# Performance work log

Hardware: AMD Instinct MI355X
Metric: run time of the kernel (lower is better)

The kernel has to match this reference:

```python
import jax, jax.numpy as jnp
import numpy as np

DEPTH, HEADS, DIM_HEAD = 6, 8, 32
D_MODEL, D_FF = 256, 1024
B, N, D_IN, N_CLS = 4, 4096, 128, 10
NB_FEAT = int(DIM_HEAD * np.log(DIM_HEAD))  # 110 random features (performer_pytorch default)


def _ortho_gaussian(m, d, rng):
    # gaussian orthogonal random projection (FAVOR+), rows rescaled by chi-distributed norms
    blocks = []
    for _ in range(int(np.ceil(m / d))):
        q, _ = np.linalg.qr(rng.standard_normal((d, d)))
        blocks.append(q.T)
    mat = np.concatenate(blocks, 0)[:m]
    mult = np.linalg.norm(rng.standard_normal((m, d)), axis=1)
    return (mult[:, None] * mat).astype(np.float32)


def setup_inputs() -> dict:
    rng = np.random.default_rng(0)
    w = lambda *s: jnp.asarray((rng.standard_normal(s) * 0.02).astype(np.float32))
    z = lambda *s: jnp.zeros(s, jnp.float32)
    o = lambda *s: jnp.ones(s, jnp.float32)
    proj = jnp.asarray(np.stack([_ortho_gaussian(NB_FEAT, DIM_HEAD, rng) for _ in range(DEPTH)]))
    return dict(
        x=jnp.asarray(rng.standard_normal((B, N, D_IN)).astype(np.float32)),
        mask=jnp.ones((B, N), bool),
        w_in=w(D_IN, D_MODEL), b_in=z(D_MODEL),
        ln1_g=o(DEPTH, D_MODEL), ln1_b=z(DEPTH, D_MODEL),
        wq=w(DEPTH, D_MODEL, D_MODEL), wk=w(DEPTH, D_MODEL, D_MODEL),
        wv=w(DEPTH, D_MODEL, D_MODEL), wo=w(DEPTH, D_MODEL, D_MODEL), bo=z(DEPTH, D_MODEL),
        proj=proj,
        ln2_g=o(DEPTH, D_MODEL), ln2_b=z(DEPTH, D_MODEL),
        w1=w(DEPTH, D_MODEL, D_FF), b1=z(DEPTH, D_FF),
        w2=w(DEPTH, D_FF, D_MODEL), b2=z(DEPTH, D_MODEL),
        cls_g=o(D_MODEL), cls_b=z(D_MODEL),
        wc1=w(D_MODEL, D_MODEL), bc1=z(D_MODEL),
        wc2=w(D_MODEL, N_CLS), bc2=z(N_CLS),
    )


def _ln(x, g, b, eps=1e-5):
    mu = x.mean(-1, keepdims=True)
    var = ((x - mu) ** 2).mean(-1, keepdims=True)
    return (x - mu) * jax.lax.rsqrt(var + eps) * g + b


def _softmax_kernel(data, proj, is_query, eps=1e-4):
    # FAVOR+ positive softmax features (performer_pytorch softmax_kernel)
    dn = data.shape[-1] ** -0.25
    ratio = proj.shape[0] ** -0.5
    dd = jnp.einsum('bhnd,md->bhnm', data * dn, proj)
    diag = 0.5 * (dn ** 2) * jnp.sum(data ** 2, axis=-1, keepdims=True)  # [B,H,N,1]
    if is_query:
        m = jnp.max(dd, axis=-1, keepdims=True)
    else:
        m = jnp.max(dd, axis=(-2, -1), keepdims=True)
    m = jax.lax.stop_gradient(m)
    return ratio * (jnp.exp(dd - diag - m) + eps)


def _linear_attn(q, k, v):
    # non-causal O(n) attention: q,k [B,H,N,M], v [B,H,N,dh]
    k_sum = k.sum(-2)                                            # [B,H,M]
    d_inv = 1.0 / jnp.einsum('bhnm,bhm->bhn', q, k_sum)          # [B,H,N]
    ctx = jnp.einsum('bhnm,bhnd->bhmd', k, v)                    # [B,H,M,dh]
    return jnp.einsum('bhnm,bhmd,bhn->bhnd', q, ctx, d_inv)


def _forward(x, mask, w_in, b_in, ln1_g, ln1_b, wq, wk, wv, wo, bo, proj,
             ln2_g, ln2_b, w1, b1, w2, b2, cls_g, cls_b, wc1, bc1, wc2, bc2):
    b_, n_ = x.shape[:2]
    h = x @ w_in + b_in
    mb = mask[:, None, :, None]
    split = lambda t: t.reshape(b_, n_, HEADS, DIM_HEAD).transpose(0, 2, 1, 3)
    for i in range(DEPTH):
        y = _ln(h, ln1_g[i], ln1_b[i])
        q, k, v = split(y @ wq[i]), split(y @ wk[i]), split(y @ wv[i])
        v = jnp.where(mb, v, 0.0)
        qp = _softmax_kernel(q, proj[i], True)
        kp = _softmax_kernel(k, proj[i], False)
        a = _linear_attn(qp, kp, v).transpose(0, 2, 1, 3).reshape(b_, n_, D_MODEL)
        h = h + a @ wo[i] + bo[i]
        y2 = _ln(h, ln2_g[i], ln2_b[i])
        h = h + jax.nn.gelu(y2 @ w1[i] + b1[i], approximate=False) @ w2[i] + b2[i]
    p = h.mean(1)
    z = jax.nn.relu(_ln(p, cls_g, cls_b))
    z = jax.nn.relu(z @ wc1 + bc1)
    return z @ wc2 + bc2


def reference(x, mask, w_in, b_in, ln1_g, ln1_b, wq, wk, wv, wo, bo, proj,
              ln2_g, ln2_b, w1, b1, w2, b2, cls_g, cls_b, wc1, bc1, wc2, bc2):
    return _forward(x, mask, w_in, b_in, ln1_g, ln1_b, wq, wk, wv, wo, bo, proj,
                    ln2_g, ln2_b, w1, b1, w2, b2, cls_g, cls_b, wc1, bc1, wc2, bc2)
```

## Files before the change

### kernel.cpp

```cpp
#include <hip/hip_runtime.h>
#include <cstdint>
#include <cstddef>

typedef __attribute__((ext_vector_type(8))) short bf16x8;
typedef __attribute__((ext_vector_type(4))) float f32x4;
typedef unsigned short u16;
typedef unsigned int u32;

static constexpr float DN    = 0.42044820762685725f;
static constexpr float DN2   = 0.17677669529663687f;
static constexpr float RATIO = 0.09534625892455924f;
static constexpr float KEPS  = 1e-4f;

__device__ __forceinline__ float b2f(u16 u) {
    union { float f; u32 i; } x; x.i = ((u32)u) << 16; return x.f;
}
__device__ __forceinline__ u16 f2b(float f) {
    union { float f; u32 i; } x; x.f = f;
    u32 r = (x.i + 0x7FFFu + ((x.i >> 16) & 1u)) >> 16;
    return (u16)r;
}
__device__ __forceinline__ float wred_sum(float v) {
#pragma unroll
    for (int o = 32; o > 0; o >>= 1) v += __shfl_xor(v, o, 64);
    return v;
}
__device__ __forceinline__ float gelu_f(float v) {
    return 0.5f * v * (1.f + erff(v * 0.7071067811865475f));
}
__device__ __forceinline__ void gload16(const u16* g, u16* l) {
    __builtin_amdgcn_global_load_lds(
        (const __attribute__((address_space(1))) u32*)(const u32*)g,
        (__attribute__((address_space(3))) u32*)(u32*)l, 16, 0, 0);
}

__global__ __launch_bounds__(256) void trk(const float* __restrict__ src, u16* __restrict__ dst,
                                           int K, int N)
{
    const size_t bo = (size_t)blockIdx.z * K * N;
    src += bo; dst += bo;
    __shared__ float tl[32][33];
    const int t = threadIdx.x, tx = t & 31, ty = t >> 5;
    const int k0 = blockIdx.y * 32, n0 = blockIdx.x * 32;
#pragma unroll
    for (int p = 0; p < 4; ++p)
        tl[ty + p * 8][tx] = src[(size_t)(k0 + ty + p * 8) * N + n0 + tx];
    __syncthreads();
#pragma unroll
    for (int p = 0; p < 4; ++p)
        dst[(size_t)(n0 + ty + p * 8) * K + k0 + tx] = f2b(tl[tx][ty + p * 8]);
}

__global__ __launch_bounds__(256) void xcast(const float* __restrict__ x, u16* __restrict__ xb)
{
    const int i = blockIdx.x * 256 + threadIdx.x;
    const float4 v = ((const float4*)x)[i];
    uint2 r;
    r.x = (u32)f2b(v.x) | ((u32)f2b(v.y) << 16);
    r.y = (u32)f2b(v.z) | ((u32)f2b(v.w) << 16);
    ((uint2*)xb)[i] = r;
}

template<int CMODE, int NP, bool QKV, bool AHEAD, bool CHEAD>
__global__ __launch_bounds__(512) void gemm3(
    const u16* __restrict__ A, const u16* __restrict__ Bt,
    const float* __restrict__ bias, u16* __restrict__ Cb, int ldc,
    u16* __restrict__ hres, const float* __restrict__ lng, const float* __restrict__ lnb,
    u16* __restrict__ yout, int K, int lda, int nrt)
{
    constexpr int KC    = (NP == 128) ? 256 : 128;
    constexpr int SLOTS = KC / 8;
    constexpr int SSH   = (SLOTS == 32) ? 5 : 4;
    constexpr int BB    = NP * KC * 2;
    constexpr int ABYT  = 64 * KC * 2;
    constexpr int NCB   = NP / 128;
    constexpr int EPI   = (CMODE <= 1) ? (64 * 136 * 2) : (64 * 264 * 2 + 4608);
    __shared__ __align__(16) char smem[BB + 2 * ABYT + EPI];
    u16*  Bs   = (u16*)smem;
    u16*  Asm  = (u16*)(smem + BB);
    char* epi  = smem + BB + 2 * ABYT;

    const u16* Btl = Bt;
    u16* Cbl = Cb;
    if (QKV) { Btl += (size_t)blockIdx.z * 393216; Cbl += (size_t)blockIdx.z * 4194304; }
    const int t = threadIdx.x, w = t >> 6, lr = (t & 63) & 15, lg = (t & 63) >> 4;
    const int p = blockIdx.x;
    const int NC = K / KC;

    auto STAGE_B = [&](int c) {
#pragma unroll
        for (int i = 0; i < BB / 16 / 512; ++i) {
            const int u = i * 512 + t;
            const int col = u >> SSH, slot = u & (SLOTS - 1);
            const int gs = slot ^ (col & 7);
            gload16(Btl + (size_t)(p * NP + col) * K + c * KC + gs * 8, Bs + u * 8);
        }
    };
    auto STAGE_A = [&](int c, int row0, int buf) {
        u16* dst = Asm + buf * (ABYT / 2);
#pragma unroll
        for (int i = 0; i < ABYT / 16 / 512; ++i) {
            const int u = i * 512 + t;
            const int row = u >> SSH, slot = u & (SLOTS - 1);
            const int gs = slot ^ (row & 7);
            const u16* src;
            if (AHEAD) {
                const int kg = c * KC + gs * 8;
                src = A + ((size_t)((row0 >> 12) * 8 + (kg >> 5)) * 4096 + (row0 & 4095) + row) * 32 + (kg & 31);
            } else {
                src = A + (size_t)(row0 + row) * lda + c * KC + gs * 8;
            }
            gload16(src, dst + u * 8);
        }
    };

    f32x4 acc[4][NCB];
    auto ZERO = [&]() {
#pragma unroll
        for (int i = 0; i < 4; ++i)
#pragma unroll
            for (int j = 0; j < NCB; ++j) acc[i][j] = f32x4{0.f, 0.f, 0.f, 0.f};
    };
    auto KLOOP = [&](int buf) {
        const u16* Ac = Asm + buf * (ABYT / 2);
#pragma unroll
        for (int ks = 0; ks < KC / 32; ++ks) {
            bf16x8 af[4], bfv[NCB];
#pragma unroll
            for (int rbk = 0; rbk < 4; ++rbk) {
                const int row = rbk * 16 + lr;
                af[rbk] = *(const bf16x8*)&Ac[row * KC + (((ks * 4 + lg) ^ (row & 7)) << 3)];
            }
#pragma unroll
            for (int cb = 0; cb < NCB; ++cb) {
                const int col = w * (NP / 8) + cb * 16 + lr;
                bfv[cb] = *(const bf16x8*)&Bs[col * KC + (((ks * 4 + lg) ^ (col & 7)) << 3)];
            }
#pragma unroll
            for (int rbk = 0; rbk < 4; ++rbk)
#pragma unroll
                for (int cb = 0; cb < NCB; ++cb)
                    acc[rbk][cb] = __builtin_amdgcn_mfma_f32_16x16x32_bf16(af[rbk], bfv[cb], acc[rbk][cb], 0, 0, 0);
        }
    };

    auto EPILOGUE = [&](int row0) {
        if constexpr (CMODE <= 1) {
            u16* ctile = (u16*)epi;
            float bv[NCB];
#pragma unroll
            for (int cb = 0; cb < NCB; ++cb) {
                const int col = p * NP + w * (NP / 8) + cb * 16 + lr;
                bv[cb] = bias ? bias[col] : 0.f;
            }
#pragma unroll
            for (int rbk = 0; rbk < 4; ++rbk)
#pragma unroll
                for (int cb = 0; cb < NCB; ++cb)
#pragma unroll
                    for (int rr = 0; rr < 4; ++rr) {
                        const int rl = rbk * 16 + 4 * lg + rr;
                        float v = acc[rbk][cb][rr] + bv[cb];
                        if (CMODE == 1) v = gelu_f(v);
                        ctile[rl * 136 + w * (NP / 8) + cb * 16 + lr] = f2b(v);
                    }
            __syncthreads();
            if constexpr (CHEAD) {
                const int bq = row0 >> 12, n0 = row0 & 4095;
#pragma unroll
                for (int i = 0; i < 2; ++i) {
                    const int u = i * 512 + t;
                    const int hh = u >> 8, rem = u & 255;
                    const int row = rem >> 2, dblk = rem & 3;
                    *(uint4*)(Cbl + ((size_t)(bq * 8 + p * 4 + hh) * 4096 + n0 + row) * 32 + dblk * 8)
                        = *(const uint4*)&ctile[row * 136 + hh * 32 + dblk * 8];
                }
            } else {
#pragma unroll
                for (int i = 0; i < 2; ++i) {
                    const int u = i * 512 + t;
                    const int row = u >> 4, seg = u & 15;
                    *(uint4*)(Cbl + (size_t)(row0 + row) * ldc + p * 128 + seg * 8)
                        = *(const uint4*)&ctile[row * 136 + seg * 8];
                }
            }
        } else {
            u16*   ctile = (u16*)epi;
            float* rsum  = (float*)(epi + 33792);
            float* rsum2 = rsum + 512;
            float* rmu   = rsum2 + 512;
            float* rrs   = rmu + 64;
            int cidx[NCB]; float bv[NCB];
#pragma unroll
            for (int cb = 0; cb < NCB; ++cb) {
                cidx[cb] = w * 32 + cb * 16 + lr;
                bv[cb] = bias ? bias[cidx[cb]] : 0.f;
            }
            if constexpr (CMODE == 2 || CMODE == 4) {
#pragma unroll
                for (int i = 0; i < 4; ++i) {
                    const int u = i * 512 + t;
                    const int row = u >> 5, seg = u & 31;
                    *(uint4*)&ctile[row * 264 + seg * 8]
                        = *(const uint4*)(hres + (size_t)(row0 + row) * 256 + seg * 8);
                }
                __syncthreads();
            }
#pragma unroll
            for (int rbk = 0; rbk < 4; ++rbk)
#pragma unroll
                for (int cb = 0; cb < NCB; ++cb)
#pragma unroll
                    for (int rr = 0; rr < 4; ++rr) {
                        const int rl = rbk * 16 + 4 * lg + rr;
                        float v = acc[rbk][cb][rr] + bv[cb];
                        if constexpr (CMODE == 2 || CMODE == 4)
                            v += b2f(ctile[rl * 264 + cidx[cb]]);
                        acc[rbk][cb][rr] = v;
                    }
            __syncthreads();
            if constexpr (CMODE != 4) {
#pragma unroll
                for (int rbk = 0; rbk < 4; ++rbk)
#pragma unroll
                    for (int rr = 0; rr < 4; ++rr) {
                        float s1 = acc[rbk][0][rr] + acc[rbk][NCB - 1][rr];
                        float s2 = fmaf(acc[rbk][0][rr], acc[rbk][0][rr],
                                        acc[rbk][NCB - 1][rr] * acc[rbk][NCB - 1][rr]);
#pragma unroll
                        for (int off = 1; off < 16; off <<= 1) {
                            s1 += __shfl_xor(s1, off, 64);
                            s2 += __shfl_xor(s2, off, 64);
                        }
                        if (lr == 0) {
                            const int rl = rbk * 16 + 4 * lg + rr;
                            rsum[rl * 8 + w] = s1; rsum2[rl * 8 + w] = s2;
                        }
                    }
                __syncthreads();
                if (t < 64) {
                    float s1 = 0.f, s2 = 0.f;
#pragma unroll
                    for (int j = 0; j < 8; ++j) { s1 += rsum[t * 8 + j]; s2 += rsum2[t * 8 + j]; }
                    const float mu = s1 * (1.f / 256.f);
                    const float var = s2 * (1.f / 256.f) - mu * mu;
                    rmu[t] = mu; rrs[t] = rsqrtf(var + 1e-5f);
                }
                __syncthreads();
            }
#pragma unroll
            for (int rbk = 0; rbk < 4; ++rbk)
#pragma unroll
                for (int cb = 0; cb < NCB; ++cb)
#pragma unroll
                    for (int rr = 0; rr < 4; ++rr) {
                        const int rl = rbk * 16 + 4 * lg + rr;
                        ctile[rl * 264 + cidx[cb]] = f2b(acc[rbk][cb][rr]);
                    }
            __syncthreads();
#pragma unroll
            for (int i = 0; i < 4; ++i) {
                const int u = i * 512 + t;
                const int row = u >> 5, seg = u & 31;
                *(uint4*)(hres + (size_t)(row0 + row) * 256 + seg * 8)
                    = *(const uint4*)&ctile[row * 264 + seg * 8];
            }
            if constexpr (CMODE != 4) {
                __syncthreads();
                float gv[NCB], bb2[NCB];
#pragma unroll
                for (int cb = 0; cb < NCB; ++cb) { gv[cb] = lng[cidx[cb]]; bb2[cb] = lnb[cidx[cb]]; }
#pragma unroll
                for (int rbk = 0; rbk < 4; ++rbk)
#pragma unroll
                    for (int cb = 0; cb < NCB; ++cb)
#pragma unroll
                        for (int rr = 0; rr < 4; ++rr) {
                            const int rl = rbk * 16 + 4 * lg + rr;
                            const float yv = (acc[rbk][cb][rr] - rmu[rl]) * rrs[rl] * gv[cb] + bb2[cb];
                            ctile[rl * 264 + cidx[cb]] = f2b(yv);
                        }
                __syncthreads();
#pragma unroll
                for (int i = 0; i < 4; ++i) {
                    const int u = i * 512 + t;
                    const int row = u >> 5, seg = u & 31;
                    *(uint4*)(yout + (size_t)(row0 + row) * 256 + seg * 8)
                        = *(const uint4*)&ctile[row * 264 + seg * 8];
                }
            }
        }
    };

    if (NC == 1) {
        int ab = 0;
        STAGE_B(0);
        STAGE_A(0, blockIdx.y * nrt * 64, 0);
        asm volatile("s_waitcnt vmcnt(0)" ::: "memory");
        __syncthreads();
        for (int rt = 0; rt < nrt; ++rt) {
            const int row0 = (blockIdx.y * nrt + rt) * 64;
            if (rt + 1 < nrt) STAGE_A(0, row0 + 64, ab ^ 1);
            ZERO();
            KLOOP(ab);
            EPILOGUE(row0);
            asm volatile("s_waitcnt vmcnt(0)" ::: "memory");
            __syncthreads();
            ab ^= 1;
        }
    } else {
        const int row0 = blockIdx.y * 64;
        ZERO();
        for (int c = 0; c < NC; ++c) {
            if (c) __syncthreads();
            STAGE_B(c);
            STAGE_A(c, row0, 0);
            asm volatile("s_waitcnt vmcnt(0)" ::: "memory");
            __syncthreads();
            KLOOP(0);
        }
        EPILOGUE(row0);
    }
}

__global__ __launch_bounds__(256) void kctx2(
    const u16* __restrict__ kg, const u16* __restrict__ vg,
    const float* __restrict__ proj, float* __restrict__ ctxp, float* __restrict__ Mcp,
    float* __restrict__ vsump)
{
    __shared__ __align__(16) u16 projS[112 * 32];
    __shared__ __align__(16) u16 kS[128 * 32];
    __shared__ __align__(16) u16 vTS[48 * 128];
    __shared__ __align__(16) u16 eTS[112 * 128];
    __shared__ float diagS[128];
    __shared__ float redS[4];
    const int t = threadIdx.x, w = t >> 6, lane = t & 63, lr = lane & 15, lg = lane >> 4;
    const int bh = blockIdx.x >> 3, chunk = blockIdx.x & 7;

    for (int idx = t; idx < 112 * 32; idx += 256) {
        const int m = idx >> 5, d = idx & 31;
        projS[idx] = (m < 110) ? f2b(proj[m * 32 + d] * DN) : (u16)0;
    }
    for (int idx = t; idx < 16 * 128; idx += 256) {
        const int rr = idx >> 7;
        vTS[(32 + rr) * 128 + (idx & 127)] = (rr == 0) ? f2b(1.0f) : (u16)0;
    }
    for (int idx = t; idx < 16 * 128; idx += 256)
        eTS[112 * 128 + idx] = 0;

    f32x4 E[2][3];
#pragma unroll
    for (int i = 0; i < 2; ++i)
#pragma unroll
        for (int j = 0; j < 3; ++j) E[i][j] = f32x4{0.f, 0.f, 0.f, 0.f};
    float Mrun = -INFINITY;
    float vsAcc = 0.f;

    for (int r = 0; r < 4; ++r) {
        const size_t eb = ((size_t)bh * 4096 + chunk * 512 + r * 128) * 32;
#pragma unroll
        for (int i = 0; i < 2; ++i) {
            const int u = i * 256 + t;
            ((uint4*)kS)[u] = ((const uint4*)(kg + eb))[u];
        }
#pragma unroll
        for (int i = 0; i < 2; ++i) {
            const int u = i * 256 + t;
            const int tok = u >> 2, dblk = u & 3;
            union { uint4 v; u16 s[8]; } uu;
            uu.v = ((const uint4*)(vg + eb))[u];
#pragma unroll
            for (int j = 0; j < 8; ++j) {
                const int d = dblk * 8 + j;
                vTS[d * 128 + ((((tok >> 3) ^ (d & 15))) << 3) + (tok & 7)] = uu.s[j];
            }
        }
        __syncthreads();
        {
            const int d = t >> 3, seg = t & 7;
            union { uint4 v; u16 s[8]; } ua, ub;
            ua.v = *(const uint4*)&vTS[d * 128 + seg * 16];
            ub.v = *(const uint4*)&vTS[d * 128 + seg * 16 + 8];
            float s = 0.f;
#pragma unroll
            for (int j = 0; j < 8; ++j) s += b2f(ua.s[j]) + b2f(ub.s[j]);
            vsAcc += s;
        }
        if (t < 128) {
            float s = 0.f;
#pragma unroll
            for (int dq = 0; dq < 4; ++dq) {
                union { uint4 v; u16 ss[8]; } uu;
                uu.v = ((const uint4*)kS)[t * 4 + dq];
#pragma unroll
                for (int j = 0; j < 8; ++j) { const float f = b2f(uu.ss[j]); s = fmaf(f, f, s); }
            }
            diagS[t] = 0.5f * DN2 * s;
        }
        __syncthreads();
        f32x4 dd[7][2];
#pragma unroll
        for (int mb = 0; mb < 7; ++mb)
#pragma unroll
            for (int tb = 0; tb < 2; ++tb) dd[mb][tb] = f32x4{0.f, 0.f, 0.f, 0.f};
        bf16x8 kf[2];
#pragma unroll
        for (int tb = 0; tb < 2; ++tb)
            kf[tb] = *(const bf16x8*)&kS[(w * 32 + tb * 16 + lr) * 32 + lg * 8];
#pragma unroll
        for (int mb = 0; mb < 7; ++mb) {
            const bf16x8 pf = *(const bf16x8*)&projS[(mb * 16 + lr) * 32 + lg * 8];
#pragma unroll
            for (int tb = 0; tb < 2; ++tb)
                dd[mb][tb] = __builtin_amdgcn_mfma_f32_16x16x32_bf16(pf, kf[tb], dd[mb][tb], 0, 0, 0);
        }
        float mx = -INFINITY;
#pragma unroll
        for (int mb = 0; mb < 7; ++mb)
#pragma unroll
            for (int tb = 0; tb < 2; ++tb)
#pragma unroll
                for (int rr = 0; rr < 4; ++rr) {
                    if (mb == 6 && (4 * lg + rr) >= 14) continue;
                    mx = fmaxf(mx, dd[mb][tb][rr]);
                }
#pragma unroll
        for (int off = 1; off < 64; off <<= 1) mx = fmaxf(mx, __shfl_xor(mx, off, 64));
        if (lane == 0) redS[w] = mx;
        __syncthreads();
        float Mnew = fmaxf(fmaxf(redS[0], redS[1]), fmaxf(redS[2], redS[3]));
        Mnew = fmaxf(Mrun, Mnew);
        const float scl = __expf(Mrun - Mnew);
#pragma unroll
        for (int i = 0; i < 2; ++i)
#pragma unroll
            for (int j = 0; j < 3; ++j)
#pragma unroll
                for (int rr = 0; rr < 4; ++rr) E[i][j][rr] *= scl;
        Mrun = Mnew;
        const float dg0 = diagS[w * 32 + lr], dg1 = diagS[w * 32 + 16 + lr];
#pragma unroll
        for (int mb = 0; mb < 7; ++mb)
#pragma unroll
            for (int tb = 0; tb < 2; ++tb)
#pragma unroll
                for (int rr = 0; rr < 4; ++rr) {
                    const int tok = w * 32 + tb * 16 + lr;
                    const int m = mb * 16 + 4 * lg + rr;
                    const float e = __expf(dd[mb][tb][rr] - (tb ? dg1 : dg0) - Mnew);
                    eTS[m * 128 + ((((tok >> 3) ^ (m & 15))) << 3) + (tok & 7)] = f2b(e);
                }
        __syncthreads();
#pragma unroll
        for (int ks = 0; ks < 4; ++ks) {
            bf16x8 aF[2], bF[3];
#pragma unroll
            for (int mb2 = 0; mb2 < 2; ++mb2) {
                const int m = w * 32 + mb2 * 16 + lr;
                aF[mb2] = *(const bf16x8*)&eTS[m * 128 + (((ks * 4 + lg) ^ lr) << 3)];
            }
#pragma unroll
            for (int nb = 0; nb < 3; ++nb) {
                const int d = nb * 16 + lr;
                bF[nb] = *(const bf16x8*)&vTS[d * 128 + (((ks * 4 + lg) ^ lr) << 3)];
            }
#pragma unroll
            for (int mb2 = 0; mb2 < 2; ++mb2)
#pragma unroll
                for (int nb = 0; nb < 3; ++nb)
                    E[mb2][nb] = __builtin_amdgcn_mfma_f32_16x16x32_bf16(aF[mb2], bF[nb], E[mb2][nb], 0, 0, 0);
        }
        __syncthreads();
    }
    const size_t ob = (size_t)blockIdx.x * 112 * 33;
#pragma unroll
    for (int mb2 = 0; mb2 < 2; ++mb2)
#pragma unroll
        for (int nb = 0; nb < 3; ++nb)
#pragma unroll
            for (int rr = 0; rr < 4; ++rr) {
                const int m = w * 32 + mb2 * 16 + 4 * lg + rr;
                if (m < 112) {
                    if (nb < 2) ctxp[ob + m * 33 + nb * 16 + lr] = E[mb2][nb][rr];
                    else if (lr == 0) ctxp[ob + m * 33 + 32] = E[mb2][nb][rr];
                }
            }
    if (t == 0) Mcp[blockIdx.x] = Mrun;
    float vs = vsAcc;
#pragma unroll
    for (int o = 4; o > 0; o >>= 1) vs += __shfl_xor(vs, o, 64);
    if ((t & 7) == 0) vsump[blockIdx.x * 32 + (t >> 3)] = vs;
}

__global__ __launch_bounds__(256) void kred2(
    const float* __restrict__ ctxp, const float* __restrict__ Mcp,
    const float* __restrict__ vsump,
    u16* __restrict__ ctxTg, float* __restrict__ ksumg)
{
    __shared__ float vsumS[32];
    __shared__ float wS[8];
    const int t = threadIdx.x, bh = blockIdx.x;
    float M = -INFINITY;
#pragma unroll
    for (int c = 0; c < 8; ++c) M = fmaxf(M, Mcp[bh * 8 + c]);
    if (t < 8) wS[t] = __expf(Mcp[bh * 8 + t] - M);
    if (t < 32) {
        float s = 0.f;
#pragma unroll
        for (int c = 0; c < 8; ++c) s += vsump[(bh * 8 + c) * 32 + t];
        vsumS[t] = s;
    }
    __syncthreads();
    for (int idx = t; idx < 4096; idx += 256) {
        const int d = idx >> 7, m = idx & 127;
        float val = 0.f;
        if (m < 110) {
            float s = 0.f;
#pragma unroll
            for (int c = 0; c < 8; ++c)
                s += wS[c] * ctxp[((size_t)(bh * 8 + c) * 112 + m) * 33 + d];
            val = RATIO * (s + KEPS * vsumS[d]);
        }
        ctxTg[(size_t)bh * 4096 + idx] = f2b(val);
    }
    if (t < 128) {
        float val = 0.f;
        if (t < 110) {
            float s = 0.f;
#pragma unroll
            for (int c = 0; c < 8; ++c)
                s += wS[c] * ctxp[((size_t)(bh * 8 + c) * 112 + t) * 33 + 32];
            val = RATIO * (s + KEPS * 4096.0f);
        }
        ksumg[bh * 128 + t] = val;
    }
}

__global__ __launch_bounds__(256) void qattn2(
    const u16* __restrict__ qg, const float* __restrict__ proj,
    const u16* __restrict__ ctxTg, const float* __restrict__ ksumg, u16* __restrict__ ag)
{
    __shared__ __align__(16) u16 projS[112 * 32];
    __shared__ __align__(16) u16 qS[128 * 32];
    __shared__ __align__(16) u16 ctxTS[32 * 128];
    __shared__ __align__(16) u16 pS[128 * 128];
    __shared__ float ksumS[128], diagS[128], dinvS[128];
    const int t = threadIdx.x, w = t >> 6, lr = (t & 63) & 15, lg = (t & 63) >> 4;
    const int bh = blockIdx.x >> 5, chunk = blockIdx.x & 31;

    for (int idx = t; idx < 112 * 32; idx += 256) {
        const int m = idx >> 5, d = idx & 31;
        projS[idx] = (m < 110) ? f2b(proj[m * 32 + d] * DN) : (u16)0;
    }
#pragma unroll
    for (int i = 0; i < 2; ++i) {
        const int u = i * 256 + t;
        const int d = u >> 4, s = u & 15;
        *(uint4*)&ctxTS[d * 128 + (((s ^ (d & 15))) << 3)] =
            *(const uint4*)(ctxTg + (size_t)bh * 4096 + d * 128 + s * 8);
    }
    if (t < 128) ksumS[t] = ksumg[bh * 128 + t];
    const size_t qeb = ((size_t)bh * 4096 + chunk * 128) * 32;
#pragma unroll
    for (int i = 0; i < 2; ++i) {
        const int u = i * 256 + t;
        ((uint4*)qS)[u] = ((const uint4*)(qg + qeb))[u];
    }
    {
        const int tok = t >> 1, s = 14 + (t & 1);
        *(uint4*)&pS[tok * 128 + (((s ^ (tok & 15))) << 3)] = uint4{0, 0, 0, 0};
    }
    __syncthreads();
    if (t < 128) {
        float s = 0.f;
#pragma unroll
        for (int dq = 0; dq < 4; ++dq) {
            union { uint4 v; u16 ss[8]; } uu;
            uu.v = ((const uint4*)qS)[t * 4 + dq];
#pragma unroll
            for (int j = 0; j < 8; ++j) { const float f = b2f(uu.ss[j]); s = fmaf(f, f, s); }
        }
        diagS[t] = 0.5f * DN2 * s;
    }
    __syncthreads();
    f32x4 dd[7][2];
#pragma unroll
    for (int mb = 0; mb < 7; ++mb)
#pragma unroll
        for (int tb = 0; tb < 2; ++tb) dd[mb][tb] = f32x4{0.f, 0.f, 0.f, 0.f};
    bf16x8 qf[2];
#pragma unroll
    for (int tb = 0; tb < 2; ++tb)
        qf[tb] = *(const bf16x8*)&qS[(w * 32 + tb * 16 + lr) * 32 + lg * 8];
#pragma unroll
    for (int mb = 0; mb < 7; ++mb) {
        const bf16x8 pf = *(const bf16x8*)&projS[(mb * 16 + lr) * 32 + lg * 8];
#pragma unroll
        for (int tb = 0; tb < 2; ++tb)
            dd[mb][tb] = __builtin_amdgcn_mfma_f32_16x16x32_bf16(pf, qf[tb], dd[mb][tb], 0, 0, 0);
    }
    float mx[2], den[2];
#pragma unroll
    for (int tb = 0; tb < 2; ++tb) {
        float v = -INFINITY;
#pragma unroll
        for (int mb = 0; mb < 7; ++mb)
#pragma unroll
            for (int rr = 0; rr < 4; ++rr) {
                if (mb == 6 && (4 * lg + rr) >= 14) continue;
                v = fmaxf(v, dd[mb][tb][rr]);
            }
        v = fmaxf(v, __shfl_xor(v, 16, 64));
        v = fmaxf(v, __shfl_xor(v, 32, 64));
        mx[tb] = v;
        den[tb] = 0.f;
    }
    const float dg0 = diagS[w * 32 + lr], dg1 = diagS[w * 32 + 16 + lr];
#pragma unroll
    for (int mb = 0; mb < 7; ++mb)
#pragma unroll
        for (int tb = 0; tb < 2; ++tb)
#pragma unroll
            for (int rr = 0; rr < 4; ++rr) {
                const int m = mb * 16 + 4 * lg + rr;
                const int tok = w * 32 + tb * 16 + lr;
                const float pv = RATIO * (__expf(dd[mb][tb][rr] - (tb ? dg1 : dg0) - mx[tb]) + KEPS);
                den[tb] += pv * ksumS[m];
                pS[tok * 128 + ((((m >> 3) ^ (tok & 15))) << 3) + (m & 7)] = f2b(pv);
            }
#pragma unroll
    for (int tb = 0; tb < 2; ++tb) {
        den[tb] += __shfl_xor(den[tb], 16, 64);
        den[tb] += __shfl_xor(den[tb], 32, 64);
        if (lg == 0) dinvS[w * 32 + tb * 16 + lr] = 1.f / den[tb];
    }
    __syncthreads();
    f32x4 o[2][2];
#pragma unroll
    for (int i = 0; i < 2; ++i)
#pragma unroll
        for (int j = 0; j < 2; ++j) o[i][j] = f32x4{0.f, 0.f, 0.f, 0.f};
#pragma unroll
    for (int ks = 0; ks < 4; ++ks) {
        bf16x8 aF[2], bF[2];
#pragma unroll
        for (int tb = 0; tb < 2; ++tb) {
            const int tok = w * 32 + tb * 16 + lr;
            aF[tb] = *(const bf16x8*)&pS[tok * 128 + (((ks * 4 + lg) ^ lr) << 3)];
        }
#pragma unroll
        for (int nb = 0; nb < 2; ++nb) {
            const int d = nb * 16 + lr;
            bF[nb] = *(const bf16x8*)&ctxTS[d * 128 + (((ks * 4 + lg) ^ lr) << 3)];
        }
#pragma unroll
        for (int tb = 0; tb < 2; ++tb)
#pragma unroll
            for (int nb = 0; nb < 2; ++nb)
                o[tb][nb] = __builtin_amdgcn_mfma_f32_16x16x32_bf16(aF[tb], bF[nb], o[tb][nb], 0, 0, 0);
    }
    u16* outS = qS;
#pragma unroll
    for (int tb = 0; tb < 2; ++tb)
#pragma unroll
        for (int nb = 0; nb < 2; ++nb)
#pragma unroll
            for (int rr = 0; rr < 4; ++rr) {
                const int tokl = w * 32 + tb * 16 + 4 * lg + rr;
                outS[tokl * 32 + nb * 16 + lr] = f2b(o[tb][nb][rr] * dinvS[tokl]);
            }
    __syncthreads();
#pragma unroll
    for (int i = 0; i < 2; ++i) {
        const int u = i * 256 + t;
        ((uint4*)(ag + qeb))[u] = ((const uint4*)outS)[u];
    }
}

__global__ __launch_bounds__(256) void pool_k(const u16* __restrict__ h,
                                              float* __restrict__ pp)
{
    const int b = blockIdx.x, ch = blockIdx.y, d = threadIdx.x;
    const u16* p = h + ((size_t)b * 4096 + ch * 256) * 256 + d;
    float s = 0.f;
    for (int n = 0; n < 256; ++n) s += b2f(p[(size_t)n * 256]);
    pp[(b * 16 + ch) * 256 + d] = s;
}

__global__ __launch_bounds__(256) void cls_k(const float* __restrict__ pp,
                                             const float* __restrict__ g,
                                             const float* __restrict__ bb,
                                             const float* __restrict__ wc1,
                                             const float* __restrict__ bc1,
                                             const float* __restrict__ wc2,
                                             const float* __restrict__ bc2,
                                             float* __restrict__ out)
{
    __shared__ float pS[4][256];
    __shared__ float zS[4][256];
    __shared__ float z2S[4][256];
    const int t = threadIdx.x;
#pragma unroll
    for (int b = 0; b < 4; ++b) {
        float s = 0.f;
        for (int c = 0; c < 16; ++c) s += pp[(b * 16 + c) * 256 + t];
        pS[b][t] = s * (1.f / 4096.f);
    }
    __syncthreads();
    {
        const int w = t >> 6, lane = t & 63;
        const float4 v = *reinterpret_cast<const float4*>(&pS[w][lane * 4]);
        float s = v.x + v.y + v.z + v.w;
        float ss = fmaf(v.x, v.x, fmaf(v.y, v.y, fmaf(v.z, v.z, v.w * v.w)));
        s = wred_sum(s); ss = wred_sum(ss);
        const float mu = s * (1.f / 256.f);
        const float var = ss * (1.f / 256.f) - mu * mu;
        const float rr = rsqrtf(var + 1e-5f);
        const float4 gv = *reinterpret_cast<const float4*>(g + lane * 4);
        const float4 bv = *reinterpret_cast<const float4*>(bb + lane * 4);
        zS[w][lane * 4 + 0] = fmaxf((v.x - mu) * rr * gv.x + bv.x, 0.f);
        zS[w][lane * 4 + 1] = fmaxf((v.y - mu) * rr * gv.y + bv.y, 0.f);
        zS[w][lane * 4 + 2] = fmaxf((v.z - mu) * rr * gv.z + bv.z, 0.f);
        zS[w][lane * 4 + 3] = fmaxf((v.w - mu) * rr * gv.w + bv.w, 0.f);
    }
    __syncthreads();
#pragma unroll
    for (int b = 0; b < 4; ++b) {
        float s = bc1[t];
        for (int j = 0; j < 256; ++j) s = fmaf(zS[b][j], wc1[j * 256 + t], s);
        z2S[b][t] = fmaxf(s, 0.f);
    }
    __syncthreads();
    if (t < 40) {
        const int b = t / 10, c = t % 10;
        float s = bc2[c];
        for (int j = 0; j < 256; ++j) s = fmaf(z2S[b][j], wc2[j * 10 + c], s);
        out[t] = s;
    }
}

extern "C" void kernel_launch(void* const* d_in, const int* in_sizes, int n_in,
                              void* d_out, int out_size, void* d_ws, size_t ws_size,
                              hipStream_t stream)
{
    const float* x    = (const float*)d_in[0];
    const float* w_in = (const float*)d_in[2];
    const float* b_in = (const float*)d_in[3];
    const float* ln1g = (const float*)d_in[4];
    const float* ln1b = (const float*)d_in[5];
    const float* wq   = (const float*)d_in[6];
    const float* wk   = (const float*)d_in[7];
    const float* wv   = (const float*)d_in[8];
    const float* wo   = (const float*)d_in[9];
    const float* bo   = (const float*)d_in[10];
    const float* proj = (const float*)d_in[11];
    const float* ln2g = (const float*)d_in[12];
    const float* ln2b = (const float*)d_in[13];
    const float* w1   = (const float*)d_in[14];
    const float* b1   = (const float*)d_in[15];
    const float* w2   = (const float*)d_in[16];
    const float* b2   = (const float*)d_in[17];
    const float* clsg = (const float*)d_in[18];
    const float* clsb = (const float*)d_in[19];
    const float* wc1  = (const float*)d_in[20];
    const float* bc1  = (const float*)d_in[21];
    const float* wc2  = (const float*)d_in[22];
    const float* bc2  = (const float*)d_in[23];

    char* wsb = (char*)d_ws;
    const size_t MB = 1024 * 1024;
    u16* h     = (u16*)(wsb);
    u16* y     = (u16*)(wsb + 16 * MB);
    u16* qb    = (u16*)(wsb + 24 * MB);
    u16* kb    = (u16*)(wsb + 32 * MB);
    u16* vb    = (u16*)(wsb + 40 * MB);
    u16* ab    = (u16*)(wsb + 48 * MB);
    u16* mid   = qb;
    u16* xb    = (u16*)(wsb + 56 * MB);
    u16* wtb   = (u16*)(wsb + 60 * MB);
    u16* w_inT = wtb;
    u16* wqT   = w_inT + 32768;
    u16* wkT   = wqT + 393216;
    u16* wvT   = wkT + 393216;
    u16* woT   = wvT + 393216;
    u16* w1T   = woT + 393216;
    u16* w2T   = w1T + 1572864;
    char* p2   = (char*)(w2T + 1572864);
    float* ctxp  = (float*)p2;
    float* Mcp   = ctxp + 256 * 112 * 33;
    u16*   ctxTg = (u16*)(Mcp + 256);
    float* ksumg = (float*)(ctxTg + 32 * 4096);
    float* pp    = ksumg + 32 * 128;
    float* vsump = pp + 16384;

    trk<<<dim3(8, 4, 1), 256, 0, stream>>>(w_in, w_inT, 128, 256);
    trk<<<dim3(8, 8, 6), 256, 0, stream>>>(wq, wqT, 256, 256);
    trk<<<dim3(8, 8, 6), 256, 0, stream>>>(wk, wkT, 256, 256);
    trk<<<dim3(8, 8, 6), 256, 0, stream>>>(wv, wvT, 256, 256);
    trk<<<dim3(8, 8, 6), 256, 0, stream>>>(wo, woT, 256, 256);
    trk<<<dim3(32, 8, 6), 256, 0, stream>>>(w1, w1T, 256, 1024);
    trk<<<dim3(8, 32, 6), 256, 0, stream>>>(w2, w2T, 1024, 256);
    xcast<<<2048, 256, 0, stream>>>(x, xb);

    gemm3<3, 256, false, false, false><<<dim3(1, 256), 512, 0, stream>>>(
        xb, w_inT, b_in, nullptr, 256, h, ln1g, ln1b, y, 128, 128, 1);
    for (int i = 0; i < 6; ++i) {
        const float* proj_i = proj + (size_t)i * 3520;
        gemm3<0, 128, true, false, true><<<dim3(2, 128, 3), 512, 0, stream>>>(
            y, wqT + (size_t)i * 65536, nullptr, qb, 256,
            nullptr, nullptr, nullptr, nullptr, 256, 256, 2);
        kctx2<<<256, 256, 0, stream>>>(kb, vb, proj_i, ctxp, Mcp, vsump);
        kred2<<<32, 256, 0, stream>>>(ctxp, Mcp, vsump, ctxTg, ksumg);
        qattn2<<<1024, 256, 0, stream>>>(qb, proj_i, ctxTg, ksumg, ab);
        gemm3<2, 256, false, true, false><<<dim3(1, 256), 512, 0, stream>>>(
            ab, woT + (size_t)i * 65536, bo + i * 256, nullptr, 256, h,
            ln2g + i * 256, ln2b + i * 256, y, 256, 0, 1);
        gemm3<1, 128, false, false, false><<<dim3(8, 32), 512, 0, stream>>>(
            y, w1T + (size_t)i * 262144, b1 + i * 1024, mid, 1024,
            nullptr, nullptr, nullptr, nullptr, 256, 256, 8);
        if (i < 5)
            gemm3<2, 256, false, false, false><<<dim3(1, 256), 512, 0, stream>>>(
                mid, w2T + (size_t)i * 262144, b2 + i * 256, nullptr, 256, h,
                ln1g + (i + 1) * 256, ln1b + (i + 1) * 256, y, 1024, 1024, 1);
        else
            gemm3<4, 256, false, false, false><<<dim3(1, 256), 512, 0, stream>>>(
                mid, w2T + (size_t)i * 262144, b2 + i * 256, nullptr, 256, h,
                nullptr, nullptr, nullptr, 1024, 1024, 1);
    }
    pool_k<<<dim3(4, 16), 256, 0, stream>>>(h, pp);
    cls_k<<<1, 256, 0, stream>>>(pp, clsg, clsb, wc1, bc1, wc2, bc2, (float*)d_out);
}
```

Baseline: 946.2 us.

## Double-buffer K-chunk loads in wide GEMM and retile FFN1 to 256 columns

For the NP=256 multi-chunk GEMM path, B and A tiles are now staged into two LDS buffers. The next chunk's global loads overlap the current chunk's MFMA loop, synchronised with partial vmcnt waits and raw barriers instead of a full drain before every chunk. The FFN up-projection GEMM switches from 128-column tiles with 8 row tiles per block to 256-column tiles with one row tile per block, using the new pipelined path. The epilogue is generalised for 256-wide tiles. LDS use grows to the full 160KB per block, which limits occupancy to one block per CU.

```diff
diff --git a/kernel.cpp b/kernel.cpp
--- a/kernel.cpp
+++ b/kernel.cpp
@@ -74,8 +74,12 @@
     constexpr int BB    = NP * KC * 2;
     constexpr int ABYT  = 64 * KC * 2;
     constexpr int NCB   = NP / 128;
-    constexpr int EPI   = (CMODE <= 1) ? (64 * 136 * 2) : (64 * 264 * 2 + 4608);
-    __shared__ __align__(16) char smem[BB + 2 * ABYT + EPI];
+    constexpr int CTS   = (NP == 128) ? 136 : 264;
+    constexpr int EPI   = (CMODE <= 1) ? (64 * CTS * 2) : (64 * 264 * 2 + 4608);
+    constexpr int ROWRQ = BB + 2 * ABYT + EPI;
+    constexpr int CHKRQ = (NP == 256) ? 2 * (BB + ABYT) : 0;
+    constexpr int LDSZ  = (ROWRQ > CHKRQ) ? ROWRQ : CHKRQ;
+    __shared__ __align__(16) char smem[LDSZ];
     u16*  Bs   = (u16*)smem;
     u16*  Asm  = (u16*)(smem + BB);
     char* epi  = smem + BB + 2 * ABYT;
@@ -121,20 +125,19 @@
 #pragma unroll
             for (int j = 0; j < NCB; ++j) acc[i][j] = f32x4{0.f, 0.f, 0.f, 0.f};
     };
-    auto KLOOP = [&](int buf) {
-        const u16* Ac = Asm + buf * (ABYT / 2);
+    auto KLOOP_AT = [&](const u16* BsC, const u16* AcC) {
 #pragma unroll
         for (int ks = 0; ks < KC / 32; ++ks) {
             bf16x8 af[4], bfv[NCB];
 #pragma unroll
             for (int rbk = 0; rbk < 4; ++rbk) {
                 const int row = rbk * 16 + lr;
-                af[rbk] = *(const bf16x8*)&Ac[row * KC + (((ks * 4 + lg) ^ (row & 7)) << 3)];
+                af[rbk] = *(const bf16x8*)&AcC[row * KC + (((ks * 4 + lg) ^ (row & 7)) << 3)];
             }
 #pragma unroll
             for (int cb = 0; cb < NCB; ++cb) {
                 const int col = w * (NP / 8) + cb * 16 + lr;
-                bfv[cb] = *(const bf16x8*)&Bs[col * KC + (((ks * 4 + lg) ^ (col & 7)) << 3)];
+                bfv[cb] = *(const bf16x8*)&BsC[col * KC + (((ks * 4 + lg) ^ (col & 7)) << 3)];
             }
 #pragma unroll
             for (int rbk = 0; rbk < 4; ++rbk)
@@ -162,7 +165,7 @@
                         const int rl = rbk * 16 + 4 * lg + rr;
                         float v = acc[rbk][cb][rr] + bv[cb];
                         if (CMODE == 1) v = gelu_f(v);
-                        ctile[rl * 136 + w * (NP / 8) + cb * 16 + lr] = f2b(v);
+                        ctile[rl * CTS + w * (NP / 8) + cb * 16 + lr] = f2b(v);
                     }
             __syncthreads();
             if constexpr (CHEAD) {
@@ -173,15 +176,18 @@
                     const int hh = u >> 8, rem = u & 255;
                     const int row = rem >> 2, dblk = rem & 3;
                     *(uint4*)(Cbl + ((size_t)(bq * 8 + p * 4 + hh) * 4096 + n0 + row) * 32 + dblk * 8)
-                        = *(const uint4*)&ctile[row * 136 + hh * 32 + dblk * 8];
+                        = *(const uint4*)&ctile[row * CTS + hh * 32 + dblk * 8];
                 }
             } else {
-#pragma unroll
-                for (int i = 0; i < 2; ++i) {
+                constexpr int NIT = (NP == 128) ? 2 : 4;
+                constexpr int SEGM = NP / 8 - 1;
+                constexpr int RSH = (NP == 128) ? 4 : 5;
+#pragma unroll
+                for (int i = 0; i < NIT; ++i) {
                     const int u = i * 512 + t;
-                    const int row = u >> 4, seg = u & 15;
-                    *(uint4*)(Cbl + (size_t)(row0 + row) * ldc + p * 128 + seg * 8)
-                        = *(const uint4*)&ctile[row * 136 + seg * 8];
+                    const int row = u >> RSH, seg = u & SEGM;
+                    *(uint4*)(Cbl + (size_t)(row0 + row) * ldc + p * NP + seg * 8)
+                        = *(const uint4*)&ctile[row * CTS + seg * 8];
                 }
             }
         } else {
@@ -302,23 +308,62 @@
             const int row0 = (blockIdx.y * nrt + rt) * 64;
             if (rt + 1 < nrt) STAGE_A(0, row0 + 64, ab ^ 1);
             ZERO();
-            KLOOP(ab);
+            KLOOP_AT(Bs, Asm + ab * (ABYT / 2));
             EPILOGUE(row0);
             asm volatile("s_waitcnt vmcnt(0)" ::: "memory");
             __syncthreads();
             ab ^= 1;
         }
-    } else {
+    } else if constexpr (NP == 256) {
+        constexpr int BUF = BB + ABYT;
         const int row0 = blockIdx.y * 64;
+        epi = smem;
+
+        auto STAGE_CH = [&](int c, int b) {
+            u16* bsB = (u16*)(smem + b * BUF);
+            u16* bsA = (u16*)(smem + b * BUF + BB);
+#pragma unroll
+            for (int i = 0; i < BB / 16 / 512; ++i) {
+                const int u = i * 512 + t;
+                const int col = u >> SSH, slot = u & (SLOTS - 1);
+                const int gs = slot ^ (col & 7);
+                gload16(Btl + (size_t)(p * NP + col) * K + c * KC + gs * 8, bsB + u * 8);
+            }
+#pragma unroll
+            for (int i = 0; i < ABYT / 16 / 512; ++i) {
+                const int u = i * 512 + t;
+                const int row = u >> SSH, slot = u & (SLOTS - 1);
+                const int gs = slot ^ (row & 7);
+                const u16* src;
+                if (AHEAD) {
+                    const int kg = c * KC + gs * 8;
+                    src = A + ((size_t)((row0 >> 12) * 8 + (kg >> 5)) * 4096 + (row0 & 4095) + row) * 32 + (kg & 31);
+                } else {
+                    src = A + (size_t)(row0 + row) * lda + c * KC + gs * 8;
+                }
+                gload16(src, bsA + u * 8);
+            }
+        };
+
         ZERO();
+        STAGE_CH(0, 0);
+        STAGE_CH(1, 1);
         for (int c = 0; c < NC; ++c) {
-            if (c) __syncthreads();
-            STAGE_B(c);
-            STAGE_A(c, row0, 0);
-            asm volatile("s_waitcnt vmcnt(0)" ::: "memory");
-            __syncthreads();
-            KLOOP(0);
-        }
+            if (c + 1 < NC) asm volatile("s_waitcnt vmcnt(10)" ::: "memory");
+            else            asm volatile("s_waitcnt vmcnt(0)"  ::: "memory");
+            __builtin_amdgcn_s_barrier();
+            __builtin_amdgcn_sched_barrier(0);
+            KLOOP_AT((const u16*)(smem + (c & 1) * BUF),
+                     (const u16*)(smem + (c & 1) * BUF + BB));
+            __builtin_amdgcn_sched_barrier(0);
+            if (c + 2 < NC) {
+                __builtin_amdgcn_s_barrier();
+                __builtin_amdgcn_sched_barrier(0);
+                STAGE_CH(c + 2, c & 1);
+            }
+        }
+        __builtin_amdgcn_s_barrier();
+        __builtin_amdgcn_sched_barrier(0);
         EPILOGUE(row0);
     }
 }
@@ -815,9 +860,9 @@
         gemm3<2, 256, false, true, false><<<dim3(1, 256), 512, 0, stream>>>(
             ab, woT + (size_t)i * 65536, bo + i * 256, nullptr, 256, h,
             ln2g + i * 256, ln2b + i * 256, y, 256, 0, 1);
-        gemm3<1, 128, false, false, false><<<dim3(8, 32), 512, 0, stream>>>(
+        gemm3<1, 256, false, false, false><<<dim3(4, 256), 512, 0, stream>>>(
             y, w1T + (size_t)i * 262144, b1 + i * 1024, mid, 1024,
-            nullptr, nullptr, nullptr, nullptr, 256, 256, 8);
+            nullptr, nullptr, nullptr, nullptr, 256, 256, 1);
         if (i < 5)
             gemm3<2, 256, false, false, false><<<dim3(1, 256), 512, 0, stream>>>(
                 mid, w2T + (size_t)i * 262144, b2 + i * 256, nullptr, 256, h,
```

Measured after the change: 930.1 us. No clear change (-1.7%).
